# Optimization experiments

Hardware: AMD Instinct MI355X
Metric: run time of the kernel (lower is better)

The kernel has to match this reference:

```python
import jax, jax.numpy as jnp
import numpy as np
import math

D_MODEL = 1024
N_HEAD = 16
Q_DIM = K_DIM = V_DIM = 1024
SCALE = math.sqrt(D_MODEL // N_HEAD)  # 8.0
B, LQ, LK = 2, 2048, 2048


def setup_inputs() -> dict:
    key = jax.random.key(0)
    ks = jax.random.split(key, 10)
    s = 1.0 / math.sqrt(Q_DIM)
    return {
        "q": jax.random.normal(ks[0], (B, LQ, Q_DIM), jnp.float32),
        "k": jax.random.normal(ks[1], (B, LK, K_DIM), jnp.float32),
        "v": jax.random.normal(ks[2], (B, LK, V_DIM), jnp.float32),
        "mask": jax.random.randint(ks[3], (B, LQ, LK), 0, 2, jnp.int32),
        "Wq": jax.random.uniform(ks[4], (D_MODEL, Q_DIM), jnp.float32, -s, s),
        "bq": jnp.zeros((D_MODEL,), jnp.float32),
        "Wk": jax.random.uniform(ks[5], (D_MODEL, K_DIM), jnp.float32, -s, s),
        "bk": jnp.zeros((D_MODEL,), jnp.float32),
        "Wv": jax.random.uniform(ks[6], (D_MODEL, V_DIM), jnp.float32, -s, s),
        "bv": jnp.zeros((D_MODEL,), jnp.float32),
    }


def reference(q, k, v, Wq, bq, Wk, bk, Wv, bv, mask):
    b, lq, _ = q.shape
    lk = k.shape[1]
    dh = D_MODEL // N_HEAD
    # linear projections (torch Linear: x @ W.T + b)
    qh = (q @ Wq.T + bq).reshape(b, lq, N_HEAD, dh).transpose(0, 2, 1, 3)  # bhqd
    kh = (k @ Wk.T + bk).reshape(b, lk, N_HEAD, dh).transpose(0, 2, 1, 3)  # bhkd
    vh = (v @ Wv.T + bv).reshape(b, lk, N_HEAD, dh).transpose(0, 2, 1, 3)  # bhkd
    attn = jnp.einsum("bhqd,bhkd->bhqk", qh, kh) / SCALE
    m = mask[:, None, :, :]  # b1qk
    attn = jnp.where(m == 0, -jnp.inf, attn)
    # rows whose mask is all-zero are reset to 0 pre-softmax (-> uniform weights)
    row_empty = (m.sum(-1, keepdims=True) == 0)
    attn = jnp.where(row_empty, 0.0, attn)
    attn = jax.nn.softmax(attn, axis=-1)  # dropout is identity in eval mode
    v_out = jnp.einsum("bhqk,bhkd->bhqd", attn, vh)
    v_out = v_out.transpose(0, 2, 1, 3).reshape(b, lq, D_MODEL)
    k_out = jnp.einsum("bhqk,bhkd->bhqd", attn, kh)
    k_out = k_out.transpose(0, 2, 1, 3).reshape(b, lq, D_MODEL)
    return (k_out, v_out)
```

## Files before the change

kernel.cpp:

```cpp
#include <hip/hip_runtime.h>
#include <hip/hip_bf16.h>
#include <stdint.h>

typedef __bf16 bf16x8 __attribute__((ext_vector_type(8)));
typedef __bf16 bf16x4 __attribute__((ext_vector_type(4)));
typedef float f32x4 __attribute__((ext_vector_type(4)));

#define B_ 2
#define LQ_ 2048
#define LK_ 2048
#define NH_ 16
#define DH_ 64
#define DM_ 1024
#define NKT_ (LK_ / 64)

#define AS1 __attribute__((address_space(1)))
#define AS3 __attribute__((address_space(3)))

__device__ __forceinline__ void gload_lds16(const void* g, void* l) {
  __builtin_amdgcn_global_load_lds((const AS1 uint32_t*)g, (AS3 uint32_t*)l, 16, 0, 0);
}

__global__ __launch_bounds__(256) void prep_kernel(
    const float* __restrict__ q, const float* __restrict__ k,
    const float* __restrict__ v, const float* __restrict__ wq,
    const float* __restrict__ wk, const float* __restrict__ wv,
    const int* __restrict__ mask,
    __bf16* __restrict__ Xt0, __bf16* __restrict__ Xt1, __bf16* __restrict__ Xt2,
    __bf16* __restrict__ Wt0, __bf16* __restrict__ Wt1, __bf16* __restrict__ Wt2,
    unsigned* __restrict__ maskp) {
  const int t = threadIdx.x;
  const int bidx = blockIdx.x;
  if (bidx >= 960) {
    int pb = bidx - 960;
    int lane = t & 63;
    size_t gi = ((size_t)pb * 256 + t) * 4;
    int4 mv = *(const int4*)(mask + gi);
    unsigned nib = (mv.x != 0 ? 1u : 0u) | (mv.y != 0 ? 2u : 0u) |
                   (mv.z != 0 ? 4u : 0u) | (mv.w != 0 ? 8u : 0u);
    unsigned vv = nib << ((lane & 7) * 4);
    vv |= __shfl_xor(vv, 1, 64);
    vv |= __shfl_xor(vv, 2, 64);
    vv |= __shfl_xor(vv, 4, 64);
    if ((lane & 7) == 0) maskp[gi >> 5] = vv;
    return;
  }
  __shared__ __align__(16) __bf16 lb[16][1032];
  const float* src; __bf16* dst; int rows, m0;
  if (bidx < 256)      { src = q;  dst = Xt0; rows = 4096; m0 = bidx * 16; }
  else if (bidx < 512) { src = k;  dst = Xt1; rows = 4096; m0 = (bidx - 256) * 16; }
  else if (bidx < 768) { src = v;  dst = Xt2; rows = 4096; m0 = (bidx - 512) * 16; }
  else if (bidx < 832) { src = wq; dst = Wt0; rows = 1024; m0 = (bidx - 768) * 16; }
  else if (bidx < 896) { src = wk; dst = Wt1; rows = 1024; m0 = (bidx - 832) * 16; }
  else                 { src = wv; dst = Wt2; rows = 1024; m0 = (bidx - 896) * 16; }
#pragma unroll
  for (int i = 0; i < 16; i++) {
    float4 f = *(const float4*)(src + (size_t)(m0 + i) * DM_ + t * 4);
    bf16x4 o;
    o[0] = (__bf16)f.x; o[1] = (__bf16)f.y; o[2] = (__bf16)f.z; o[3] = (__bf16)f.w;
    *(bf16x4*)&lb[i][t * 4] = o;
  }
  __syncthreads();
  const int wave = t >> 6, lane = t & 63;
  const int m = lane >> 2, c = lane & 3;
#pragma unroll
  for (int j = 0; j < 8; j++) {
    int kt = wave * 8 + j;
    bf16x8 val = *(const bf16x8*)&lb[m][kt * 32 + (c ^ (m & 3)) * 8];
    *(bf16x8*)(dst + ((size_t)kt * rows + m0 + m) * 32 + c * 8) = val;
  }
}

__global__ __launch_bounds__(256) void proj_kernel(
    const __bf16* __restrict__ Xt0, const __bf16* __restrict__ Xt1,
    const __bf16* __restrict__ Xt2,
    const float* __restrict__ b0p, const float* __restrict__ b1p,
    const float* __restrict__ b2p,
    const __bf16* __restrict__ Wt0, const __bf16* __restrict__ Wt1,
    const __bf16* __restrict__ Wt2,
    __bf16* __restrict__ qh, __bf16* __restrict__ kh,
    __bf16* __restrict__ khT, __bf16* __restrict__ vhT) {
  __shared__ __align__(16) __bf16 smem[2][2][128 * 32];
  __bf16* cbuf = &smem[0][0][0];

  const int mode = blockIdx.z;
  const __bf16* Xt = mode == 0 ? Xt0 : (mode == 1 ? Xt1 : Xt2);
  const __bf16* Wt = mode == 0 ? Wt0 : (mode == 1 ? Wt1 : Wt2);
  const float* bias = mode == 0 ? b0p : (mode == 1 ? b1p : b2p);
  __bf16* ostd = mode == 0 ? qh : (mode == 1 ? kh : nullptr);
  __bf16* otr = mode == 0 ? nullptr : (mode == 1 ? khT : vhT);
  const float osc = mode == 0 ? 0.18033688f : 1.0f;

  const int t = threadIdx.x;
  const int wave = t >> 6, lane = t & 63;
  const int lo16 = lane & 15, quad = lane >> 4;
  const int wm = wave >> 1, wn = wave & 1;
  const int m0 = blockIdx.x * 128, n0 = blockIdx.y * 128;

  f32x4 acc[4][4] = {};

  auto stage = [&](int kt, int sel) {
#pragma unroll
    for (int ii = 2 * wave; ii < 2 * wave + 2; ii++) {
      gload_lds16(Xt + ((size_t)kt * 4096 + m0 + ii * 16) * 32 + lane * 8,
                  &smem[sel][0][ii * 512]);
      gload_lds16(Wt + ((size_t)kt * 1024 + n0 + ii * 16) * 32 + lane * 8,
                  &smem[sel][1][ii * 512]);
    }
  };

  stage(0, 0);
  for (int kt = 0; kt < 32; kt++) {
    const int sel = kt & 1;
    __syncthreads();
    if (kt + 1 < 32) stage(kt + 1, sel ^ 1);
    bf16x8 af[4], bfr[4];
#pragma unroll
    for (int g = 0; g < 4; g++) {
      int ar = wm * 64 + g * 16 + lo16;
      af[g] = *(const bf16x8*)(&smem[sel][0][ar * 32 + (quad ^ (ar & 3)) * 8]);
      int br = wn * 64 + g * 16 + lo16;
      bfr[g] = *(const bf16x8*)(&smem[sel][1][br * 32 + (quad ^ (br & 3)) * 8]);
    }
#pragma unroll
    for (int gm = 0; gm < 4; gm++)
#pragma unroll
      for (int gn = 0; gn < 4; gn++)
        acc[gm][gn] =
            __builtin_amdgcn_mfma_f32_16x16x32_bf16(af[gm], bfr[gn], acc[gm][gn], 0, 0, 0);
  }

  const int b = m0 >> 11, l0 = m0 & 2047;
  for (int nhf = 0; nhf < 2; nhf++) {
    int h = (n0 >> 6) + nhf;
    int bh = b * NH_ + h;
    if (ostd) {
      __syncthreads();
      if (wn == nhf) {
#pragma unroll
        for (int gn = 0; gn < 4; gn++) {
          float bi = bias[n0 + nhf * 64 + gn * 16 + lo16];
#pragma unroll
          for (int gm = 0; gm < 4; gm++)
#pragma unroll
            for (int r = 0; r < 4; r++)
              cbuf[(wm * 64 + gm * 16 + quad * 4 + r) * 72 + gn * 16 + lo16] =
                  (__bf16)((acc[gm][gn][r] + bi) * osc);
        }
      }
      __syncthreads();
      int m = t >> 1, coff = (t & 1) * 32;
      __bf16* dst = ostd + ((size_t)bh * LQ_ + l0 + m) * DH_ + coff;
#pragma unroll
      for (int j = 0; j < 4; j++)
        *(bf16x8*)(dst + j * 8) = *(const bf16x8*)&cbuf[m * 72 + coff + j * 8];
    }
    if (otr) {
      __syncthreads();
      if (wn == nhf) {
#pragma unroll
        for (int gn = 0; gn < 4; gn++) {
          float bi = bias[n0 + nhf * 64 + gn * 16 + lo16];
#pragma unroll
          for (int gm = 0; gm < 4; gm++) {
            bf16x4 pk;
#pragma unroll
            for (int r = 0; r < 4; r++) pk[r] = (__bf16)(acc[gm][gn][r] + bi);
            *(bf16x4*)&cbuf[(gn * 16 + lo16) * 136 + wm * 64 + gm * 16 + quad * 4] = pk;
          }
        }
      }
      __syncthreads();
      int d = t >> 2, mc = (t & 3) * 32;
      int kti = (l0 + mc) >> 6, kl = (l0 + mc) & 63;
      __bf16* dst = otr + ((size_t)(bh * NKT_ + kti) * 64 + d) * 64 + kl;
#pragma unroll
      for (int j = 0; j < 4; j++)
        *(bf16x8*)(dst + j * 8) = *(const bf16x8*)&cbuf[d * 136 + mc + j * 8];
    }
  }
}

__global__ __launch_bounds__(512) void attn_kernel(
    const __bf16* __restrict__ qh, const __bf16* __restrict__ kh,
    const __bf16* __restrict__ khT, const __bf16* __restrict__ vhT,
    const unsigned* __restrict__ maskp,
    float* __restrict__ out_k, float* __restrict__ out_v) {
  __shared__ __align__(16) __bf16 kbuf[2][64 * 64];
  __shared__ __align__(16) __bf16 ktbuf[2][64 * 64];
  __shared__ __align__(16) __bf16 vtbuf[2][64 * 64];
  __shared__ __align__(16) __bf16 p_lds[8][16][72];

  const int t = threadIdx.x;
  const int wave = t >> 6, lane = t & 63;
  const int lo16 = lane & 15, quad = lane >> 4;
  const int bh = blockIdx.x;
  const int b = bh >> 4, h = bh & 15;
  const int q0 = blockIdx.y * 128 + wave * 16;
  const int srow = lane >> 3;
  const int scg = (lane & 7) ^ srow;
  const int rsw = lo16 & 7;

  bf16x8 a_q0, a_q1;
  {
    const __bf16* qrow = qh + ((size_t)bh * LQ_ + q0 + lo16) * DH_ + quad * 8;
    a_q0 = *(const bf16x8*)(qrow);
    a_q1 = *(const bf16x8*)(qrow + 32);
  }

  bf16x8 ones;
#pragma unroll
  for (int j = 0; j < 8; j++) ones[j] = (__bf16)1.0f;

  f32x4 acc_v[4] = {};
  f32x4 acc_k[4] = {};
  f32x4 acc_l = {};

  const __bf16* khb = kh + (size_t)bh * LK_ * DH_;
  const __bf16* ktb = khT + (size_t)bh * LK_ * DH_;
  const __bf16* vtb = vhT + (size_t)bh * LK_ * DH_;

  const int row_s = wave * 8 + srow;
  auto stage = [&](int kti, int sel) {
    const int tb = kti * 4096;
    gload_lds16(khb + (size_t)(kti * 64 + row_s) * DH_ + scg * 8, &kbuf[sel][wave * 512]);
    gload_lds16(ktb + tb + row_s * 64 + scg * 8, &ktbuf[sel][wave * 512]);
    gload_lds16(vtb + tb + row_s * 64 + scg * 8, &vtbuf[sel][wave * 512]);
  };

  stage(0, 0);
  for (int kti = 0; kti < NKT_; kti++) {
    const int cur = kti & 1;
    __syncthreads();
    if (kti + 1 < NKT_) stage(kti + 1, cur ^ 1);

    const unsigned* mb =
        maskp + ((size_t)b * LQ_ + q0 + lo16) * (LK_ / 32) + kti * 2;
    unsigned mw0 = mb[0], mw1 = mb[1];

    __builtin_amdgcn_s_setprio(1);
    f32x4 s[4];
#pragma unroll
    for (int gg = 0; gg < 4; gg++) {
      int row = gg * 16 + lo16;
      bf16x8 kb0 = *(const bf16x8*)(&kbuf[cur][row * 64 + ((quad ^ rsw) * 8)]);
      bf16x8 kb1 = *(const bf16x8*)(&kbuf[cur][row * 64 + (((quad + 4) ^ rsw) * 8)]);
      f32x4 z = {};
      z = __builtin_amdgcn_mfma_f32_16x16x32_bf16(kb0, a_q0, z, 0, 0, 0);
      z = __builtin_amdgcn_mfma_f32_16x16x32_bf16(kb1, a_q1, z, 0, 0, 0);
      s[gg] = z;
    }
    __builtin_amdgcn_s_setprio(0);

#pragma unroll
    for (int gg = 0; gg < 4; gg++) {
      unsigned w = (gg >= 2) ? mw1 : mw0;
      bf16x4 pk;
#pragma unroll
      for (int r = 0; r < 4; r++) {
        int bitpos = (gg & 1) * 16 + quad * 4 + r;
        float pe = __builtin_amdgcn_exp2f(s[gg][r]);
        pk[r] = ((w >> bitpos) & 1) ? (__bf16)pe : (__bf16)0.0f;
      }
      *(bf16x4*)&p_lds[wave][lo16][gg * 16 + quad * 4] = pk;
    }
    bf16x8 a_p0 = *(const bf16x8*)&p_lds[wave][lo16][quad * 8];
    bf16x8 a_p1 = *(const bf16x8*)&p_lds[wave][lo16][32 + quad * 8];

    __builtin_amdgcn_s_setprio(1);
#pragma unroll
    for (int gg = 0; gg < 4; gg++) {
      int row = gg * 16 + lo16;
      bf16x8 bv0 = *(const bf16x8*)(&vtbuf[cur][row * 64 + ((quad ^ rsw) * 8)]);
      bf16x8 bv1 = *(const bf16x8*)(&vtbuf[cur][row * 64 + (((quad + 4) ^ rsw) * 8)]);
      bf16x8 bk0 = *(const bf16x8*)(&ktbuf[cur][row * 64 + ((quad ^ rsw) * 8)]);
      bf16x8 bk1 = *(const bf16x8*)(&ktbuf[cur][row * 64 + (((quad + 4) ^ rsw) * 8)]);
      acc_v[gg] = __builtin_amdgcn_mfma_f32_16x16x32_bf16(a_p0, bv0, acc_v[gg], 0, 0, 0);
      acc_v[gg] = __builtin_amdgcn_mfma_f32_16x16x32_bf16(a_p1, bv1, acc_v[gg], 0, 0, 0);
      acc_k[gg] = __builtin_amdgcn_mfma_f32_16x16x32_bf16(a_p0, bk0, acc_k[gg], 0, 0, 0);
      acc_k[gg] = __builtin_amdgcn_mfma_f32_16x16x32_bf16(a_p1, bk1, acc_k[gg], 0, 0, 0);
    }
    acc_l = __builtin_amdgcn_mfma_f32_16x16x32_bf16(a_p0, ones, acc_l, 0, 0, 0);
    acc_l = __builtin_amdgcn_mfma_f32_16x16x32_bf16(a_p1, ones, acc_l, 0, 0, 0);
    __builtin_amdgcn_s_setprio(0);
  }

  float inv_l[4];
#pragma unroll
  for (int r = 0; r < 4; r++) inv_l[r] = 1.0f / acc_l[r];
  size_t obase = ((size_t)b * LQ_ + q0 + quad * 4) * DM_ + h * DH_;
#pragma unroll
  for (int gg = 0; gg < 4; gg++) {
#pragma unroll
    for (int r = 0; r < 4; r++) {
      size_t idx = obase + (size_t)r * DM_ + gg * 16 + lo16;
      out_k[idx] = acc_k[gg][r] * inv_l[r];
      out_v[idx] = acc_v[gg][r] * inv_l[r];
    }
  }
}

extern "C" void kernel_launch(void* const* d_in, const int* in_sizes, int n_in,
                              void* d_out, int out_size, void* d_ws, size_t ws_size,
                              hipStream_t stream) {
  const float* q = (const float*)d_in[0];
  const float* k = (const float*)d_in[1];
  const float* v = (const float*)d_in[2];
  const int* mask = (const int*)d_in[3];
  const float* Wq = (const float*)d_in[4];
  const float* bq = (const float*)d_in[5];
  const float* Wk = (const float*)d_in[6];
  const float* bk = (const float*)d_in[7];
  const float* Wv = (const float*)d_in[8];
  const float* bv = (const float*)d_in[9];
  float* out = (float*)d_out;

  const size_t HTOT = (size_t)B_ * NH_ * LQ_ * DH_;
  const size_t XTOT = (size_t)B_ * LQ_ * DM_;
  const size_t MASKW = (size_t)B_ * LQ_ * (LK_ / 32);
  __bf16* qh = (__bf16*)d_ws;
  __bf16* kh = qh + HTOT;
  __bf16* khT = kh + HTOT;
  __bf16* vhT = khT + HTOT;
  unsigned* maskp = (unsigned*)(vhT + HTOT);

  const size_t SCR_ELEMS = 3 * XTOT + 3 * (size_t)DM_ * DM_;
  const size_t NEED = 4 * HTOT * sizeof(__bf16) + MASKW * sizeof(unsigned) +
                      SCR_ELEMS * sizeof(__bf16);
  __bf16* scr = (ws_size >= NEED) ? (__bf16*)(maskp + MASKW) : (__bf16*)d_out;
  __bf16* Xt0 = scr;
  __bf16* Xt1 = Xt0 + XTOT;
  __bf16* Xt2 = Xt1 + XTOT;
  __bf16* Wt0 = Xt2 + XTOT;
  __bf16* Wt1 = Wt0 + (size_t)DM_ * DM_;
  __bf16* Wt2 = Wt1 + (size_t)DM_ * DM_;

  prep_kernel<<<960 + 8192, 256, 0, stream>>>(
      q, k, v, Wq, Wk, Wv, mask, Xt0, Xt1, Xt2, Wt0, Wt1, Wt2, maskp);
  proj_kernel<<<dim3(32, 8, 3), 256, 0, stream>>>(
      Xt0, Xt1, Xt2, bq, bk, bv, Wt0, Wt1, Wt2, qh, kh, khT, vhT);
  attn_kernel<<<dim3(32, 16), 512, 0, stream>>>(qh, kh, khT, vhT, maskp,
                                                out, out + (size_t)B_ * LQ_ * DM_);
}
```

Before: 257.5 us.

## Pair waves on 32-row query tiles, splitting key and output columns

Waves are regrouped into pairs. Each pair shares a 32-query-row tile, and within the pair each wave computes half of the 64 key columns for S and half of the 64 head dims for the outputs. Each wave now reuses every K/V LDS fragment across two query sub-blocks, which halves the LDS reads per MFMA. The price is a second __syncthreads per key tile so the P halves can be exchanged through shared memory, and the next-tile prefetch now issues later in the loop, which shortens load/compute overlap.

```diff
diff --git a/kernel.cpp b/kernel.cpp
--- a/kernel.cpp
+++ b/kernel.cpp
@@ -189,32 +189,36 @@
   __shared__ __align__(16) __bf16 kbuf[2][64 * 64];
   __shared__ __align__(16) __bf16 ktbuf[2][64 * 64];
   __shared__ __align__(16) __bf16 vtbuf[2][64 * 64];
-  __shared__ __align__(16) __bf16 p_lds[8][16][72];
+  __shared__ __align__(16) __bf16 p_lds[4][32][72];
 
   const int t = threadIdx.x;
   const int wave = t >> 6, lane = t & 63;
   const int lo16 = lane & 15, quad = lane >> 4;
+  const int tw = wave & 1;
+  const int qs = wave >> 1;
   const int bh = blockIdx.x;
   const int b = bh >> 4, h = bh & 15;
-  const int q0 = blockIdx.y * 128 + wave * 16;
+  const int q0 = blockIdx.y * 128 + qs * 32;
   const int srow = lane >> 3;
   const int scg = (lane & 7) ^ srow;
   const int rsw = lo16 & 7;
 
-  bf16x8 a_q0, a_q1;
-  {
-    const __bf16* qrow = qh + ((size_t)bh * LQ_ + q0 + lo16) * DH_ + quad * 8;
-    a_q0 = *(const bf16x8*)(qrow);
-    a_q1 = *(const bf16x8*)(qrow + 32);
+  bf16x8 a_q0[2], a_q1[2];
+#pragma unroll
+  for (int qb = 0; qb < 2; qb++) {
+    const __bf16* qrow =
+        qh + ((size_t)bh * LQ_ + q0 + qb * 16 + lo16) * DH_ + quad * 8;
+    a_q0[qb] = *(const bf16x8*)(qrow);
+    a_q1[qb] = *(const bf16x8*)(qrow + 32);
   }
 
   bf16x8 ones;
 #pragma unroll
   for (int j = 0; j < 8; j++) ones[j] = (__bf16)1.0f;
 
-  f32x4 acc_v[4] = {};
-  f32x4 acc_k[4] = {};
-  f32x4 acc_l = {};
+  f32x4 acc_v[2][2] = {};
+  f32x4 acc_k[2][2] = {};
+  f32x4 acc_l[2] = {};
 
   const __bf16* khb = kh + (size_t)bh * LK_ * DH_;
   const __bf16* ktb = khT + (size_t)bh * LK_ * DH_;
@@ -232,70 +236,101 @@
   for (int kti = 0; kti < NKT_; kti++) {
     const int cur = kti & 1;
     __syncthreads();
+
+    unsigned mw[2];
+#pragma unroll
+    for (int qb = 0; qb < 2; qb++)
+      mw[qb] = maskp[((size_t)b * LQ_ + q0 + qb * 16 + lo16) * (LK_ / 32) +
+                     kti * 2 + tw];
+
+    __builtin_amdgcn_s_setprio(1);
+    f32x4 s[2][2];
+#pragma unroll
+    for (int gg = 0; gg < 2; gg++) {
+      int krow = tw * 32 + gg * 16 + lo16;
+      bf16x8 kb0 = *(const bf16x8*)(&kbuf[cur][krow * 64 + ((quad ^ rsw) * 8)]);
+      bf16x8 kb1 = *(const bf16x8*)(&kbuf[cur][krow * 64 + (((quad + 4) ^ rsw) * 8)]);
+#pragma unroll
+      for (int qb = 0; qb < 2; qb++) {
+        f32x4 z = {};
+        z = __builtin_amdgcn_mfma_f32_16x16x32_bf16(kb0, a_q0[qb], z, 0, 0, 0);
+        z = __builtin_amdgcn_mfma_f32_16x16x32_bf16(kb1, a_q1[qb], z, 0, 0, 0);
+        s[qb][gg] = z;
+      }
+    }
+    __builtin_amdgcn_s_setprio(0);
+
+#pragma unroll
+    for (int qb = 0; qb < 2; qb++)
+#pragma unroll
+      for (int gg = 0; gg < 2; gg++) {
+        bf16x4 pk;
+#pragma unroll
+        for (int r = 0; r < 4; r++) {
+          int bitpos = gg * 16 + quad * 4 + r;
+          float pe = __builtin_amdgcn_exp2f(s[qb][gg][r]);
+          pk[r] = ((mw[qb] >> bitpos) & 1) ? (__bf16)pe : (__bf16)0.0f;
+        }
+        *(bf16x4*)&p_lds[qs][qb * 16 + lo16][tw * 32 + gg * 16 + quad * 4] = pk;
+      }
+
+    __syncthreads();
+
+    bf16x8 a_p[2][2];
+#pragma unroll
+    for (int qb = 0; qb < 2; qb++)
+#pragma unroll
+      for (int kh = 0; kh < 2; kh++)
+        a_p[qb][kh] =
+            *(const bf16x8*)&p_lds[qs][qb * 16 + lo16][kh * 32 + quad * 8];
+
     if (kti + 1 < NKT_) stage(kti + 1, cur ^ 1);
 
-    const unsigned* mb =
-        maskp + ((size_t)b * LQ_ + q0 + lo16) * (LK_ / 32) + kti * 2;
-    unsigned mw0 = mb[0], mw1 = mb[1];
-
     __builtin_amdgcn_s_setprio(1);
-    f32x4 s[4];
-#pragma unroll
-    for (int gg = 0; gg < 4; gg++) {
-      int row = gg * 16 + lo16;
-      bf16x8 kb0 = *(const bf16x8*)(&kbuf[cur][row * 64 + ((quad ^ rsw) * 8)]);
-      bf16x8 kb1 = *(const bf16x8*)(&kbuf[cur][row * 64 + (((quad + 4) ^ rsw) * 8)]);
-      f32x4 z = {};
-      z = __builtin_amdgcn_mfma_f32_16x16x32_bf16(kb0, a_q0, z, 0, 0, 0);
-      z = __builtin_amdgcn_mfma_f32_16x16x32_bf16(kb1, a_q1, z, 0, 0, 0);
-      s[gg] = z;
-    }
+#pragma unroll
+    for (int gg = 0; gg < 2; gg++) {
+      int rowd = tw * 32 + gg * 16 + lo16;
+      bf16x8 bv[2], bk[2];
+#pragma unroll
+      for (int kh = 0; kh < 2; kh++) {
+        int ch = ((quad + kh * 4) ^ rsw) * 8;
+        bv[kh] = *(const bf16x8*)(&vtbuf[cur][rowd * 64 + ch]);
+        bk[kh] = *(const bf16x8*)(&ktbuf[cur][rowd * 64 + ch]);
+      }
+#pragma unroll
+      for (int qb = 0; qb < 2; qb++)
+#pragma unroll
+        for (int kh = 0; kh < 2; kh++) {
+          acc_v[qb][gg] = __builtin_amdgcn_mfma_f32_16x16x32_bf16(
+              a_p[qb][kh], bv[kh], acc_v[qb][gg], 0, 0, 0);
+          acc_k[qb][gg] = __builtin_amdgcn_mfma_f32_16x16x32_bf16(
+              a_p[qb][kh], bk[kh], acc_k[qb][gg], 0, 0, 0);
+        }
+    }
+#pragma unroll
+    for (int qb = 0; qb < 2; qb++)
+#pragma unroll
+      for (int kh = 0; kh < 2; kh++)
+        acc_l[qb] = __builtin_amdgcn_mfma_f32_16x16x32_bf16(
+            a_p[qb][kh], ones, acc_l[qb], 0, 0, 0);
     __builtin_amdgcn_s_setprio(0);
-
-#pragma unroll
-    for (int gg = 0; gg < 4; gg++) {
-      unsigned w = (gg >= 2) ? mw1 : mw0;
-      bf16x4 pk;
+  }
+
+#pragma unroll
+  for (int qb = 0; qb < 2; qb++) {
+    float inv_l[4];
+#pragma unroll
+    for (int r = 0; r < 4; r++) inv_l[r] = 1.0f / acc_l[qb][r];
+    size_t obase =
+        ((size_t)b * LQ_ + q0 + qb * 16 + quad * 4) * DM_ + h * DH_ + tw * 32;
+#pragma unroll
+    for (int gg = 0; gg < 2; gg++) {
 #pragma unroll
       for (int r = 0; r < 4; r++) {
-        int bitpos = (gg & 1) * 16 + quad * 4 + r;
-        float pe = __builtin_amdgcn_exp2f(s[gg][r]);
-        pk[r] = ((w >> bitpos) & 1) ? (__bf16)pe : (__bf16)0.0f;
-      }
-      *(bf16x4*)&p_lds[wave][lo16][gg * 16 + quad * 4] = pk;
-    }
-    bf16x8 a_p0 = *(const bf16x8*)&p_lds[wave][lo16][quad * 8];
-    bf16x8 a_p1 = *(const bf16x8*)&p_lds[wave][lo16][32 + quad * 8];
-
-    __builtin_amdgcn_s_setprio(1);
-#pragma unroll
-    for (int gg = 0; gg < 4; gg++) {
-      int row = gg * 16 + lo16;
-      bf16x8 bv0 = *(const bf16x8*)(&vtbuf[cur][row * 64 + ((quad ^ rsw) * 8)]);
-      bf16x8 bv1 = *(const bf16x8*)(&vtbuf[cur][row * 64 + (((quad + 4) ^ rsw) * 8)]);
-      bf16x8 bk0 = *(const bf16x8*)(&ktbuf[cur][row * 64 + ((quad ^ rsw) * 8)]);
-      bf16x8 bk1 = *(const bf16x8*)(&ktbuf[cur][row * 64 + (((quad + 4) ^ rsw) * 8)]);
-      acc_v[gg] = __builtin_amdgcn_mfma_f32_16x16x32_bf16(a_p0, bv0, acc_v[gg], 0, 0, 0);
-      acc_v[gg] = __builtin_amdgcn_mfma_f32_16x16x32_bf16(a_p1, bv1, acc_v[gg], 0, 0, 0);
-      acc_k[gg] = __builtin_amdgcn_mfma_f32_16x16x32_bf16(a_p0, bk0, acc_k[gg], 0, 0, 0);
-      acc_k[gg] = __builtin_amdgcn_mfma_f32_16x16x32_bf16(a_p1, bk1, acc_k[gg], 0, 0, 0);
-    }
-    acc_l = __builtin_amdgcn_mfma_f32_16x16x32_bf16(a_p0, ones, acc_l, 0, 0, 0);
-    acc_l = __builtin_amdgcn_mfma_f32_16x16x32_bf16(a_p1, ones, acc_l, 0, 0, 0);
-    __builtin_amdgcn_s_setprio(0);
-  }
-
-  float inv_l[4];
-#pragma unroll
-  for (int r = 0; r < 4; r++) inv_l[r] = 1.0f / acc_l[r];
-  size_t obase = ((size_t)b * LQ_ + q0 + quad * 4) * DM_ + h * DH_;
-#pragma unroll
-  for (int gg = 0; gg < 4; gg++) {
-#pragma unroll
-    for (int r = 0; r < 4; r++) {
-      size_t idx = obase + (size_t)r * DM_ + gg * 16 + lo16;
-      out_k[idx] = acc_k[gg][r] * inv_l[r];
-      out_v[idx] = acc_v[gg][r] * inv_l[r];
+        size_t idx = obase + (size_t)r * DM_ + gg * 16 + lo16;
+        out_k[idx] = acc_k[qb][gg][r] * inv_l[r];
+        out_v[idx] = acc_v[qb][gg][r] * inv_l[r];
+      }
     }
   }
 }
```

New measurement: 289.9 us. 12.6% more time.
